# Optimization experiments

Measured on AMD Instinct MI355X. Metric: run time of the kernel, lower is better.

Reference implementation:

```python
import jax, jax.numpy as jnp
import numpy as np

WS = 8
NUM_HEADS = 4
DIM = 64
H = W = 128
B = 16
EPS = 1e-5


def _rel_pos_index(ws):
    coords = np.stack(np.meshgrid(np.arange(ws), np.arange(ws), indexing='ij'))  # (2,ws,ws)
    cf = coords.reshape(2, -1)
    rel = (cf[:, :, None] - cf[:, None, :]).transpose(1, 2, 0).astype(np.int64)
    rel[..., 0] += ws - 1
    rel[..., 1] += ws - 1
    rel[..., 0] *= 2 * ws - 1
    return jnp.asarray(rel.sum(-1))  # (ws*ws, ws*ws)

_RPI = _rel_pos_index(WS)


def _ln_hw(x, g, b):
    # LayerNorm over last two dims (H,W) of (B,C,H,W), affine shape (H,W)
    mu = x.mean(axis=(-2, -1), keepdims=True)
    var = ((x - mu) ** 2).mean(axis=(-2, -1), keepdims=True)
    return (x - mu) / jnp.sqrt(var + EPS) * g + b


def _ln_c(x, g, b):
    mu = x.mean(-1, keepdims=True)
    var = ((x - mu) ** 2).mean(-1, keepdims=True)
    return (x - mu) / jnp.sqrt(var + EPS) * g + b


def _win_part(x, ws):
    # (B,C,H,W) -> (B*nW, ws*ws, C)
    b, c, hh, ww = x.shape
    x = x.reshape(b, c, hh // ws, ws, ww // ws, ws)
    return x.transpose(0, 2, 4, 3, 5, 1).reshape(b * (hh // ws) * (ww // ws), ws * ws, c)


def _win_rev(w, ws, hh, ww, b):
    # (B*nW, ws*ws, C) -> (B,C,H,W)
    c = w.shape[-1]
    w = w.reshape(b, hh // ws, ww // ws, ws, ws, c)
    return w.transpose(0, 5, 1, 3, 2, 4).reshape(b, c, hh, ww)


def _forward(x, lclg1_ln1_g, lclg1_ln1_b, lclg1_conv_w, lclg1_conv_b, lclg1_ln2_g, lclg1_ln2_b,
             lclg2_ln1_g, lclg2_ln1_b, lclg2_conv_w, lclg2_conv_b, lclg2_ln2_g, lclg2_ln2_b,
             pos1, pos2, q_w, q_b, kv_w, kv_b, rpb_table, gamma, proj_w, proj_b,
             norm2_g, norm2_b, fc1_w, fc1_b, fc2_w, fc2_b):
    b, c, hh, ww = x.shape
    h = NUM_HEADS
    hd = c // h
    n = WS * WS
    scale = hd ** -0.5

    def lclg(z, g1, b1, cw, cb, g2, b2):
        z = _ln_hw(z, g1, b1)
        z = jnp.einsum('oc,bchw->bohw', cw, z) + cb[None, :, None, None]  # 1x1 conv
        return jax.nn.gelu(_ln_hw(z, g2, b2), approximate=False)

    x1 = lclg(x, lclg1_ln1_g, lclg1_ln1_b, lclg1_conv_w, lclg1_conv_b, lclg1_ln2_g, lclg1_ln2_b)
    x2 = lclg(x, lclg2_ln1_g, lclg2_ln1_b, lclg2_conv_w, lclg2_conv_b, lclg2_ln2_g, lclg2_ln2_b)

    x1w = _win_part(x1, WS) + pos1  # (B_, N, C)
    x2w = _win_part(x2, WS) + pos2
    bw = x1w.shape[0]

    q = (x1w @ q_w.T + q_b).reshape(bw, n, h, hd).transpose(0, 2, 1, 3) * scale  # (B_,h,N,hd)
    kv = (x2w @ kv_w.T + kv_b).reshape(bw, n, 2, h, hd).transpose(2, 0, 3, 1, 4)
    k, v = kv[0], kv[1]

    attn = jnp.einsum('bhnd,bhmd->bhnm', q, k)
    bias = rpb_table[_RPI.reshape(-1)].reshape(n, n, h).transpose(2, 0, 1)  # (h,N,N)
    attn = jax.nn.softmax(attn + bias[None], axis=-1)
    o = jnp.einsum('bhnm,bhmd->bhnd', attn, v)  # (B_,h,N,hd)

    # LAM_Module: attention over head_dim channels of (B_,h,N,hd)
    y = o.transpose(0, 3, 1, 2).reshape(bw, hd, h * n)  # (B_,hd,h*N)
    energy = jnp.einsum('bik,bjk->bij', y, y)  # (B_,hd,hd)
    lam = jnp.einsum('bij,bjk->bik', jax.nn.softmax(energy, axis=-1), y)
    y = (gamma * lam + y).reshape(bw, hd, h, n).transpose(0, 2, 3, 1)  # (B_,h,N,hd)

    xo = y.transpose(0, 2, 1, 3).reshape(bw, n, c) + q.transpose(0, 2, 1, 3).reshape(bw, n, c) + x1w
    xo = xo @ proj_w.T + proj_b

    xo = _win_rev(xo, WS, hh, ww, b)  # (B,C,H,W)

    # MLP with pre-norm residual over channel dim
    t = xo.reshape(b, c, hh * ww).transpose(0, 2, 1)  # (B,HW,C)
    tn = _ln_c(t, norm2_g, norm2_b)
    t = t + (jax.nn.gelu(tn @ fc1_w.T + fc1_b, approximate=False) @ fc2_w.T + fc2_b)
    return t.transpose(0, 2, 1).reshape(b, c, hh, ww)


def setup_inputs() -> dict:
    key = jax.random.key(0)
    ks = jax.random.split(key, 16)
    d = DIM

    def rn(i, shape, sc=0.02):
        return jax.random.normal(ks[i], shape, jnp.float32) * sc

    return dict(
        x=jax.random.normal(ks[0], (B, d, H, W), jnp.float32),
        lclg1_ln1_g=jnp.ones((H, W), jnp.float32), lclg1_ln1_b=jnp.zeros((H, W), jnp.float32),
        lclg1_conv_w=rn(1, (d, d)), lclg1_conv_b=jnp.zeros((d,), jnp.float32),
        lclg1_ln2_g=jnp.ones((H, W), jnp.float32), lclg1_ln2_b=jnp.zeros((H, W), jnp.float32),
        lclg2_ln1_g=jnp.ones((H, W), jnp.float32), lclg2_ln1_b=jnp.zeros((H, W), jnp.float32),
        lclg2_conv_w=rn(2, (d, d)), lclg2_conv_b=jnp.zeros((d,), jnp.float32),
        lclg2_ln2_g=jnp.ones((H, W), jnp.float32), lclg2_ln2_b=jnp.zeros((H, W), jnp.float32),
        pos1=jnp.ones((1, WS * WS, d), jnp.float32),
        pos2=jnp.ones((1, WS * WS, d), jnp.float32),
        q_w=rn(3, (d, d)), q_b=jnp.zeros((d,), jnp.float32),
        kv_w=rn(4, (2 * d, d)), kv_b=jnp.zeros((2 * d,), jnp.float32),
        rpb_table=rn(5, ((2 * WS - 1) ** 2, NUM_HEADS)),
        gamma=jnp.full((1,), 0.1, jnp.float32),
        proj_w=rn(6, (d, d)), proj_b=jnp.zeros((d,), jnp.float32),
        norm2_g=jnp.ones((d,), jnp.float32), norm2_b=jnp.zeros((d,), jnp.float32),
        fc1_w=rn(7, (d, d)), fc1_b=jnp.zeros((d,), jnp.float32),
        fc2_w=rn(8, (d, d)), fc2_b=jnp.zeros((d,), jnp.float32),
    )


def reference(x, lclg1_ln1_g, lclg1_ln1_b, lclg1_conv_w, lclg1_conv_b, lclg1_ln2_g, lclg1_ln2_b,
              lclg2_ln1_g, lclg2_ln1_b, lclg2_conv_w, lclg2_conv_b, lclg2_ln2_g, lclg2_ln2_b,
              pos1, pos2, q_w, q_b, kv_w, kv_b, rpb_table, gamma, proj_w, proj_b,
              norm2_g, norm2_b, fc1_w, fc1_b, fc2_w, fc2_b):
    return _forward(x, lclg1_ln1_g, lclg1_ln1_b, lclg1_conv_w, lclg1_conv_b, lclg1_ln2_g, lclg1_ln2_b,
                    lclg2_ln1_g, lclg2_ln1_b, lclg2_conv_w, lclg2_conv_b, lclg2_ln2_g, lclg2_ln2_b,
                    pos1, pos2, q_w, q_b, kv_w, kv_b, rpb_table, gamma, proj_w, proj_b,
                    norm2_g, norm2_b, fc1_w, fc1_b, fc2_w, fc2_b)
```

## Files before the change

kernel.cpp:

```cpp
#include <hip/hip_runtime.h>
#include <hip/hip_bf16.h>

typedef __hip_bfloat16 bf16;
typedef __attribute__((ext_vector_type(8))) short short8;
typedef __attribute__((ext_vector_type(4))) short short4v;
typedef __attribute__((ext_vector_type(4))) float float4v;
typedef __attribute__((ext_vector_type(2))) float float2v;

__device__ __forceinline__ short f2bs(float f){
    union { bf16 h; short s; } u; u.h = __float2bfloat16(f); return u.s;
}
__device__ __forceinline__ float bs2f(short s){
    return __uint_as_float(((unsigned)(unsigned short)s) << 16);
}
__device__ __forceinline__ float gelu_exact(float x){
    return 0.5f * x * (1.0f + erff(x * 0.70710678118654752440f));
}
#define MFMA(a,b,c) __builtin_amdgcn_mfma_f32_16x16x32_bf16((a),(b),(c),0,0,0)

#define HW 16384
#define NPLANE 1048576
#define EPS 1e-5f
#define LS 72

#define OFF_W1   0
#define OFF_W2   4096
#define OFF_QW   8192
#define OFF_KVW  12288
#define OFF_PW   20480
#define OFF_FW1  24576
#define OFF_FW2  28672

__global__ __launch_bounds__(256) void k_pre(const float* __restrict__ x,
                                             float* __restrict__ mu,
                                             float* __restrict__ rinv,
                                             const float* __restrict__ w1, const float* __restrict__ w2,
                                             const float* __restrict__ qw, const float* __restrict__ kvw,
                                             const float* __restrict__ pw, const float* __restrict__ fw1,
                                             const float* __restrict__ fw2,
                                             short* __restrict__ wb, float* __restrict__ rowsum){
    int bi = blockIdx.x;
    int tid = threadIdx.x;
    if (bi < 1024){
        const float* p = x + (size_t)bi * HW;
        float s = 0.f, ss = 0.f;
        for (int i = tid; i < HW/4; i += 256){
            float4v v = *(const float4v*)(p + i*4);
            #pragma unroll
            for (int k = 0; k < 4; k++){ s += v[k]; ss += v[k]*v[k]; }
        }
        __shared__ float rs[256], rss[256];
        rs[tid] = s; rss[tid] = ss; __syncthreads();
        for (int st = 128; st > 0; st >>= 1){
            if (tid < st){ rs[tid] += rs[tid+st]; rss[tid] += rss[tid+st]; }
            __syncthreads();
        }
        if (tid == 0){
            float m = rs[0] * (1.f/HW);
            float v = rss[0] * (1.f/HW) - m*m;
            mu[bi] = m; rinv[bi] = rsqrtf(v + EPS);
        }
    } else if (bi < 1032){
        int wi = bi - 1024;
        const float* src = wi==0?w1: wi==1?w2: wi==2?qw: wi==3?kvw: wi==4?(kvw+4096): wi==5?pw: wi==6?fw1: fw2;
        short* dst = wb + wi*4096;
        int base = tid*16;
        short8 o8[2];
        #pragma unroll
        for (int k = 0; k < 2; k++){
            float4v v0 = *(const float4v*)(src + base + 8*k);
            float4v v1 = *(const float4v*)(src + base + 8*k + 4);
            #pragma unroll
            for (int j = 0; j < 4; j++){ o8[k][j] = f2bs(v0[j]); o8[k][4+j] = f2bs(v1[j]); }
        }
        *(short8*)&dst[base]     = o8[0];
        *(short8*)&dst[base + 8] = o8[1];
    } else {
        if (tid < 128){
            int br = tid >> 6, o = tid & 63;
            const float* W = br ? w2 : w1;
            float s = 0.f;
            for (int c = 0; c < 64; c++) s += W[o*64 + c];
            rowsum[br*64 + o] = s;
        }
    }
}

__global__ __launch_bounds__(256) void k_conv(const float* __restrict__ x,
                                              const float* __restrict__ mu,
                                              const float* __restrict__ rinv,
                                              const float* __restrict__ g1a, const float* __restrict__ b1a,
                                              const float* __restrict__ cb1,
                                              const float* __restrict__ g1b, const float* __restrict__ b1b,
                                              const float* __restrict__ cb2,
                                              const short* __restrict__ wb,
                                              const float* __restrict__ rowsum,
                                              float* __restrict__ y1, float* __restrict__ w2g,
                                              float* __restrict__ partS, float* __restrict__ partQ){
    int blk = blockIdx.x;
    int b = blk >> 8; int tile = blk & 255; int hw0 = tile * 64;
    __shared__ __align__(16) short xn_bf[64*LS];
    const int tid = threadIdx.x;
    const int wq = tid >> 6, lane = tid & 63, qd = lane >> 4, col = lane & 15;
    const float4v zf = {0.f,0.f,0.f,0.f};

    {
        int p = tid & 63, cq = tid >> 6;
        const float* xb = x + (size_t)(b*64 + 16*cq)*HW + hw0 + p;
        float4v m4[4], r4[4];
        #pragma unroll
        for (int k = 0; k < 4; k++){
            m4[k] = *(const float4v*)(mu   + b*64 + 16*cq + 4*k);
            r4[k] = *(const float4v*)(rinv + b*64 + 16*cq + 4*k);
        }
        short8 o8[2];
        #pragma unroll
        for (int k = 0; k < 2; k++)
            #pragma unroll
            for (int j = 0; j < 8; j++){
                int jj = 8*k + j;
                float v = xb[(size_t)jj*HW];
                o8[k][j] = f2bs((v - m4[jj>>2][jj&3]) * r4[jj>>2][jj&3]);
            }
        *(short8*)&xn_bf[p*LS + 16*cq]     = o8[0];
        *(short8*)&xn_bf[p*LS + 16*cq + 8] = o8[1];
    }
    __syncthreads();

    #pragma unroll
    for (int br = 0; br < 2; br++){
        const short* W  = wb + (br ? OFF_W2 : OFF_W1);
        const float* cb = br ? cb2 : cb1;
        const float* gp = br ? g1b : g1a;
        const float* bp = br ? b1b : b1a;
        short8 a0 = *(const short8*)&W[(16*wq + col)*64 + 8*qd];
        short8 a1 = *(const short8*)&W[(16*wq + col)*64 + 32 + 8*qd];
        float cbv[4], rsv[4];
        #pragma unroll
        for (int r = 0; r < 4; r++){
            int o = 16*wq + 4*qd + r;
            cbv[r] = cb[o]; rsv[r] = rowsum[br*64 + o];
        }
        float sa[4]  = {0.f,0.f,0.f,0.f};
        float ssa[4] = {0.f,0.f,0.f,0.f};
        #pragma unroll
        for (int jn = 0; jn < 4; jn++){
            short8 bx0 = *(const short8*)&xn_bf[(16*jn + col)*LS + 8*qd];
            short8 bx1 = *(const short8*)&xn_bf[(16*jn + col)*LS + 32 + 8*qd];
            float4v acc = zf;
            acc = MFMA(a0, bx0, acc);
            acc = MFMA(a1, bx1, acc);
            int hw = hw0 + 16*jn + col;
            float gl = gp[hw], bl = bp[hw];
            float vals[4];
            #pragma unroll
            for (int r = 0; r < 4; r++){
                vals[r] = gl*acc[r] + bl*rsv[r] + cbv[r];
                sa[r]  += vals[r];
                ssa[r] += vals[r]*vals[r];
            }
            if (br == 0){
                #pragma unroll
                for (int r = 0; r < 4; r++)
                    y1[(size_t)(b*64 + 16*wq + 4*qd + r)*HW + hw] = vals[r];
            } else {
                int row = hw >> 7, cc = hw & 127;
                int win = (row >> 3)*16 + (cc >> 3);
                int t   = (row & 7)*8 + (cc & 7);
                float4v vv;
                #pragma unroll
                for (int r = 0; r < 4; r++) vv[r] = vals[r];
                *(float4v*)(w2g + ((size_t)(b*256 + win)*64 + t)*64 + 16*wq + 4*qd) = vv;
            }
        }
        #pragma unroll
        for (int r = 0; r < 4; r++){
            float s = sa[r], ss = ssa[r];
            s += __shfl_xor(s, 1); ss += __shfl_xor(ss, 1);
            s += __shfl_xor(s, 2); ss += __shfl_xor(ss, 2);
            s += __shfl_xor(s, 4); ss += __shfl_xor(ss, 4);
            s += __shfl_xor(s, 8); ss += __shfl_xor(ss, 8);
            if (col == 0){
                int o = 16*wq + 4*qd + r;
                size_t pi = ((size_t)(br*16 + b)*64 + o)*256 + tile;
                partS[pi] = s; partQ[pi] = ss;
            }
        }
    }
}

__global__ __launch_bounds__(256) void k_fin(const float* __restrict__ partS,
                                             const float* __restrict__ partQ,
                                             float* __restrict__ mu2,
                                             float* __restrict__ rinv2){
    int i = blockIdx.x*256 + threadIdx.x;
    const float* ps = partS + (size_t)i*256;
    const float* pq = partQ + (size_t)i*256;
    float s = 0.f, ss = 0.f;
    for (int k = 0; k < 64; k++){
        float4v a = *(const float4v*)(ps + k*4);
        float4v b = *(const float4v*)(pq + k*4);
        s += a[0]+a[1]+a[2]+a[3];
        ss += b[0]+b[1]+b[2]+b[3];
    }
    float m = s * (1.f/HW);
    float v = ss * (1.f/HW) - m*m;
    mu2[i] = m; rinv2[i] = rsqrtf(v + EPS);
}

__global__ __launch_bounds__(256, 4) void k_attn(float* __restrict__ x1, const float* __restrict__ w2g,
                                              const float* __restrict__ mu2, const float* __restrict__ rinv2,
                                              const float* __restrict__ g2a, const float* __restrict__ b2a,
                                              const float* __restrict__ g2b, const float* __restrict__ b2b,
                                              const float* __restrict__ pos1, const float* __restrict__ pos2,
                                              const short* __restrict__ wb,
                                              const float* __restrict__ qb, const float* __restrict__ kvb,
                                              const float* __restrict__ rpb, const float* __restrict__ gammap,
                                              const float* __restrict__ pb,
                                              const float* __restrict__ n2g, const float* __restrict__ n2b,
                                              const float* __restrict__ fb1,
                                              const float* __restrict__ fb2){
    int B = blockIdx.x;
    int hy = (B & 7) | ((B >> 5) & 8);
    int wx = (((B >> 9) & 7) << 1) | ((B >> 3) & 1);
    int b  = (B >> 4) & 15;
    int win = hy*16 + wx;

    const short* qwb  = wb + OFF_QW;
    const short* kvwb = wb + OFF_KVW;
    const short* pwb  = wb + OFF_PW;
    const short* f1b  = wb + OFF_FW1;
    const short* f2b  = wb + OFF_FW2;

    __shared__ __align__(16) char smem[40464];
    short* bufA = (short*)smem;
    short* bufK = (short*)(smem + 9216);
    short* bufV = (short*)(smem + 18432);
    short* bufQ = (short*)(smem + 27648);
    float* rpb_lds = (float*)(smem + 36864);
    float* energyS = (float*)(smem + 36864);
    short* soft_bf = (short*)(smem + 37888);
    float* XOf  = (float*)(smem + 18432);
    short* tnb  = (short*)smem;
    short* h1b  = (short*)(smem + 9216);
    float* sumS = (float*)(smem + 36864);
    float* sqS  = (float*)(smem + 37888);
    float* muS  = (float*)(smem + 38912);
    float* rinvS= (float*)(smem + 39168);

    const int tid = threadIdx.x;
    const int wq = tid >> 6, lane = tid & 63, qd = lane >> 4, col = lane & 15;
    size_t base = (size_t)b * NPLANE;
    #define HWOF(t) ((hy*8 + ((t)>>3))*128 + wx*8 + ((t)&7))

    const float4v zf = {0.f,0.f,0.f,0.f};
    const short8 zero8 = {0,0,0,0,0,0,0,0};

    for (int i = tid; i < 900; i += 256) rpb_lds[i] = rpb[i];

    {
        const float* src = w2g + ((size_t)(b*256 + win) << 12);
        int t = tid >> 2, c0 = (tid & 3) << 4;
        int hw = HWOF(t);
        float g = g2b[hw], lb = b2b[hw];
        const float* mup = mu2   + 1024 + b*64 + c0;
        const float* rvp = rinv2 + 1024 + b*64 + c0;
        short8 o8[2];
        #pragma unroll
        for (int k = 0; k < 4; k++){
            float4v v  = *(const float4v*)(src + (size_t)t*64 + c0 + 4*k);
            float4v m4 = *(const float4v*)(mup + 4*k);
            float4v r4 = *(const float4v*)(rvp + 4*k);
            float4v p4 = *(const float4v*)(pos2 + t*64 + c0 + 4*k);
            #pragma unroll
            for (int j = 0; j < 4; j++){
                float z = (v[j] - m4[j]) * r4[j] * g + lb;
                o8[k>>1][(k&1)*4 + j] = f2bs(gelu_exact(z) + p4[j]);
            }
        }
        *(short8*)&bufA[t*LS + c0]     = o8[0];
        *(short8*)&bufA[t*LS + c0 + 8] = o8[1];
    }
    __syncthreads();

    {
        short8 ax0 = *(const short8*)&bufA[(16*wq + col)*LS + 8*qd];
        short8 ax1 = *(const short8*)&bufA[(16*wq + col)*LS + 32 + 8*qd];
        #pragma unroll
        for (int jn = 0; jn < 4; jn++){
            int c = 16*jn + col;
            short8 wv0 = *(const short8*)&kvwb[(64 + c)*64 + 8*qd];
            short8 wv1 = *(const short8*)&kvwb[(64 + c)*64 + 32 + 8*qd];
            float4v acc = zf;
            acc = MFMA(ax0, wv0, acc);
            acc = MFMA(ax1, wv1, acc);
            float bv = kvb[64 + c];
            short4v pk;
            #pragma unroll
            for (int r = 0; r < 4; r++) pk[r] = f2bs(acc[r] + bv);
            *(short4v*)&bufV[c*LS + 16*wq + 4*qd] = pk;
        }
        short8 a0 = *(const short8*)&kvwb[(16*wq + col)*64 + 8*qd];
        short8 a1 = *(const short8*)&kvwb[(16*wq + col)*64 + 32 + 8*qd];
        float kbr[4];
        #pragma unroll
        for (int r = 0; r < 4; r++) kbr[r] = kvb[16*wq + 4*qd + r];
        #pragma unroll
        for (int jn = 0; jn < 4; jn++){
            int t = 16*jn + col;
            short8 bx0 = *(const short8*)&bufA[t*LS + 8*qd];
            short8 bx1 = *(const short8*)&bufA[t*LS + 32 + 8*qd];
            float4v acc = zf;
            acc = MFMA(a0, bx0, acc);
            acc = MFMA(a1, bx1, acc);
            short4v pk;
            #pragma unroll
            for (int r = 0; r < 4; r++) pk[r] = f2bs(acc[r] + kbr[r]);
            *(short4v*)&bufK[t*LS + 16*wq + 4*qd] = pk;
        }
    }
    __syncthreads();

    {
        int t = tid & 63, cq = tid >> 6;
        int hw = HWOF(t);
        float g = g2a[hw], lb = b2a[hw];
        const float* mup = mu2   + b*64 + 16*cq;
        const float* rvp = rinv2 + b*64 + 16*cq;
        float4v m4[4], r4[4], p4[4];
        #pragma unroll
        for (int k = 0; k < 4; k++){
            m4[k] = *(const float4v*)(mup + 4*k);
            r4[k] = *(const float4v*)(rvp + 4*k);
            p4[k] = *(const float4v*)(pos1 + t*64 + 16*cq + 4*k);
        }
        short8 o8[2];
        #pragma unroll
        for (int k = 0; k < 2; k++)
            #pragma unroll
            for (int j = 0; j < 8; j++){
                int jj = 8*k + j;
                float v = x1[base + (size_t)(16*cq + jj)*HW + hw];
                float z = (v - m4[jj>>2][jj&3]) * r4[jj>>2][jj&3] * g + lb;
                o8[k][j] = f2bs(gelu_exact(z) + p4[jj>>2][jj&3]);
            }
        *(short8*)&bufA[t*LS + 16*cq]     = o8[0];
        *(short8*)&bufA[t*LS + 16*cq + 8] = o8[1];
    }
    __syncthreads();

    {
        short8 a0 = *(const short8*)&qwb[(16*wq + col)*64 + 8*qd];
        short8 a1 = *(const short8*)&qwb[(16*wq + col)*64 + 32 + 8*qd];
        float qbr[4];
        #pragma unroll
        for (int r = 0; r < 4; r++) qbr[r] = qb[16*wq + 4*qd + r];
        #pragma unroll
        for (int jn = 0; jn < 4; jn++){
            int t = 16*jn + col;
            short8 bx0 = *(const short8*)&bufA[t*LS + 8*qd];
            short8 bx1 = *(const short8*)&bufA[t*LS + 32 + 8*qd];
            float4v acc = zf;
            acc = MFMA(a0, bx0, acc);
            acc = MFMA(a1, bx1, acc);
            short4v pk;
            #pragma unroll
            for (int r = 0; r < 4; r++) pk[r] = f2bs((acc[r] + qbr[r]) * 0.25f);
            *(short4v*)&bufQ[t*LS + 16*wq + 4*qd] = pk;
        }
    }
    short4v xreg[4];
    #pragma unroll
    for (int h = 0; h < 4; h++){
        short4v xr;
        #pragma unroll
        for (int r = 0; r < 4; r++)
            xr[r] = bufA[(16*wq + 4*qd + r)*LS + 16*h + col];
        xreg[h] = xr;
    }
    __syncthreads();

    int idx_t[4][4];
    {
        int t = 16*wq + col, ty = t >> 3, tx = t & 7;
        #pragma unroll
        for (int jn = 0; jn < 4; jn++)
            #pragma unroll
            for (int r = 0; r < 4; r++){
                int u = 16*jn + 4*qd + r;
                idx_t[jn][r] = (ty - (u>>3) + 7)*15 + (tx - (u&7) + 7);
            }
    }

    for (int h = 0; h < 4; h++){
        short8 bq = *(const short8*)&bufQ[(16*wq + col)*LS + h*16 + (qd & 1)*8];
        float pr[4][4];
        #pragma unroll
        for (int jn = 0; jn < 4; jn++){
            short8 ak = *(const short8*)&bufK[(16*jn + col)*LS + h*16 + (qd & 1)*8];
            if (qd >= 2) ak = zero8;
            float4v acc = MFMA(ak, bq, zf);
            #pragma unroll
            for (int r = 0; r < 4; r++)
                pr[jn][r] = acc[r] + rpb_lds[idx_t[jn][r]*4 + h];
        }
        float m = pr[0][0];
        #pragma unroll
        for (int jn = 0; jn < 4; jn++)
            #pragma unroll
            for (int r = 0; r < 4; r++) m = fmaxf(m, pr[jn][r]);
        m = fmaxf(m, __shfl_xor(m, 16));
        m = fmaxf(m, __shfl_xor(m, 32));
        float s = 0.f;
        #pragma unroll
        for (int jn = 0; jn < 4; jn++)
            #pragma unroll
            for (int r = 0; r < 4; r++){ pr[jn][r] = __expf(pr[jn][r] - m); s += pr[jn][r]; }
        s += __shfl_xor(s, 16);
        s += __shfl_xor(s, 32);
        float rc = 1.f / s;
        #pragma unroll
        for (int jn = 0; jn < 4; jn++){
            short4v pk;
            #pragma unroll
            for (int r = 0; r < 4; r++) pk[r] = f2bs(pr[jn][r] * rc);
            *(short4v*)&bufA[(16*wq + col)*LS + 16*jn + 4*qd] = pk;
        }
        short8 ap0 = *(const short8*)&bufA[(16*wq + col)*LS + 8*qd];
        short8 ap1 = *(const short8*)&bufA[(16*wq + col)*LS + 32 + 8*qd];
        short8 bv0 = *(const short8*)&bufV[(h*16 + col)*LS + 8*qd];
        short8 bv1 = *(const short8*)&bufV[(h*16 + col)*LS + 32 + 8*qd];
        float4v acc_o = zf;
        acc_o = MFMA(ap0, bv0, acc_o);
        acc_o = MFMA(ap1, bv1, acc_o);
        __syncthreads();
        short4v ot;
        #pragma unroll
        for (int r = 0; r < 4; r++) ot[r] = f2bs(acc_o[r]);
        *(short4v*)&bufV[(h*16 + col)*LS + 16*wq + 4*qd] = ot;
        #pragma unroll
        for (int r = 0; r < 4; r++)
            bufK[(16*wq + 4*qd + r)*LS + h*16 + col] = ot[r];
    }
    __syncthreads();

    {
        float4v acc_e = zf;
        #pragma unroll
        for (int h = 0; h < 4; h++){
            short8 f0 = *(const short8*)&bufV[(h*16 + col)*LS + 8*qd];
            short8 f1 = *(const short8*)&bufV[(h*16 + col)*LS + 32 + 8*qd];
            acc_e = MFMA(f0, f0, acc_e);
            acc_e = MFMA(f1, f1, acc_e);
        }
        if (wq == 0){
            #pragma unroll
            for (int r = 0; r < 4; r++) energyS[(4*qd + r)*16 + col] = acc_e[r];
        }
    }
    __syncthreads();
    if (tid < 16){
        int i = tid; float m = -1e30f;
        for (int j = 0; j < 16; j++) m = fmaxf(m, energyS[i*16 + j]);
        float s = 0.f; float e[16];
        for (int j = 0; j < 16; j++){ e[j] = __expf(energyS[i*16 + j] - m); s += e[j]; }
        float rc = 1.f / s;
        for (int j = 0; j < 16; j++) soft_bf[i*32 + j] = f2bs(e[j] * rc);
        for (int j = 0; j < 16; j++) soft_bf[i*32 + 16 + j] = 0;
    }
    __syncthreads();

    {
        float gam = gammap[0];
        short8 asf = *(const short8*)&soft_bf[col*32 + 8*qd];
        #pragma unroll
        for (int h = 0; h < 4; h++){
            short8 ay = *(const short8*)&bufK[(16*wq + col)*LS + 16*h + (qd & 1)*8];
            float4v acc = MFMA(ay, asf, zf);
            short4v xv = xreg[h];
            #pragma unroll
            for (int r = 0; r < 4; r++){
                int ro = (16*wq + 4*qd + r)*LS + 16*h + col;
                float ot = bs2f(bufK[ro]);
                float qv = bs2f(bufQ[ro]);
                float xo = gam*acc[r] + ot + qv + bs2f(xv[r]);
                bufK[ro] = f2bs(xo);
            }
        }
    }
    __syncthreads();

    {
        short8 a0 = *(const short8*)&pwb[(16*wq + col)*64 + 8*qd];
        short8 a1 = *(const short8*)&pwb[(16*wq + col)*64 + 32 + 8*qd];
        float pbr[4];
        #pragma unroll
        for (int r = 0; r < 4; r++) pbr[r] = pb[16*wq + 4*qd + r];
        #pragma unroll
        for (int jn = 0; jn < 4; jn++){
            int t = 16*jn + col;
            short8 bx0 = *(const short8*)&bufK[t*LS + 8*qd];
            short8 bx1 = *(const short8*)&bufK[t*LS + 32 + 8*qd];
            float4v acc = zf;
            acc = MFMA(a0, bx0, acc);
            acc = MFMA(a1, bx1, acc);
            float2v w0 = {acc[0]+pbr[0], acc[1]+pbr[1]};
            float2v w1 = {acc[2]+pbr[2], acc[3]+pbr[3]};
            *(float2v*)&XOf[t*66 + 16*wq + 4*qd]     = w0;
            *(float2v*)&XOf[t*66 + 16*wq + 4*qd + 2] = w1;
        }
    }
    __syncthreads();

    {
        int p = tid & 63, qg = tid >> 6;
        float s = 0.f, ss = 0.f;
        #pragma unroll
        for (int j = 0; j < 8; j++){
            float2v v = *(const float2v*)&XOf[p*66 + qg*16 + 2*j];
            s += v[0]+v[1]; ss += v[0]*v[0] + v[1]*v[1];
        }
        sumS[qg*64 + p] = s; sqS[qg*64 + p] = ss;
    }
    __syncthreads();
    if (tid < 64){
        float s  = sumS[tid] + sumS[64+tid] + sumS[128+tid] + sumS[192+tid];
        float ss = sqS[tid]  + sqS[64+tid]  + sqS[128+tid]  + sqS[192+tid];
        float m = s * (1.f/64.f);
        float var = ss * (1.f/64.f) - m*m;
        muS[tid] = m; rinvS[tid] = rsqrtf(var + EPS);
    }
    __syncthreads();
    {
        int p = tid & 63, qg = tid >> 6;
        float m = muS[p], rv = rinvS[p];
        short8 o8[2];
        #pragma unroll
        for (int k = 0; k < 2; k++)
            #pragma unroll
            for (int j = 0; j < 8; j++){
                int c = qg*16 + k*8 + j;
                o8[k][j] = f2bs((XOf[p*66 + c] - m) * rv * n2g[c] + n2b[c]);
            }
        *(short8*)&tnb[p*LS + qg*16]     = o8[0];
        *(short8*)&tnb[p*LS + qg*16 + 8] = o8[1];
    }
    __syncthreads();
    {
        short8 a0 = *(const short8*)&f1b[(16*wq + col)*64 + 8*qd];
        short8 a1 = *(const short8*)&f1b[(16*wq + col)*64 + 32 + 8*qd];
        float fbr[4];
        #pragma unroll
        for (int r = 0; r < 4; r++) fbr[r] = fb1[16*wq + 4*qd + r];
        #pragma unroll
        for (int jn = 0; jn < 4; jn++){
            int t = 16*jn + col;
            short8 bx0 = *(const short8*)&tnb[t*LS + 8*qd];
            short8 bx1 = *(const short8*)&tnb[t*LS + 32 + 8*qd];
            float4v acc = zf;
            acc = MFMA(a0, bx0, acc);
            acc = MFMA(a1, bx1, acc);
            short4v pk;
            #pragma unroll
            for (int r = 0; r < 4; r++) pk[r] = f2bs(gelu_exact(acc[r] + fbr[r]));
            *(short4v*)&h1b[t*LS + 16*wq + 4*qd] = pk;
        }
    }
    __syncthreads();
    {
        short8 a0 = *(const short8*)&h1b[(16*wq + col)*LS + 8*qd];
        short8 a1 = *(const short8*)&h1b[(16*wq + col)*LS + 32 + 8*qd];
        #pragma unroll
        for (int jn = 0; jn < 4; jn++){
            int c2 = 16*jn + col;
            short8 f0 = *(const short8*)&f2b[c2*64 + 8*qd];
            short8 f1 = *(const short8*)&f2b[c2*64 + 32 + 8*qd];
            float4v acc = zf;
            acc = MFMA(a0, f0, acc);
            acc = MFMA(a1, f1, acc);
            float bv = fb2[c2];
            float4v ov;
            #pragma unroll
            for (int r = 0; r < 4; r++)
                ov[r] = acc[r] + bv + XOf[(16*wq + 4*qd + r)*66 + c2];
            int t0 = 16*wq + 4*qd;
            *(float4v*)(x1 + base + (size_t)c2*HW + HWOF(t0)) = ov;
        }
    }
    #undef HWOF
}

extern "C" void kernel_launch(void* const* d_in, const int* in_sizes, int n_in,
                              void* d_out, int out_size, void* d_ws, size_t ws_size,
                              hipStream_t stream){
    const float* x        = (const float*)d_in[0];
    const float* l1_g1    = (const float*)d_in[1];
    const float* l1_b1    = (const float*)d_in[2];
    const float* l1_cw    = (const float*)d_in[3];
    const float* l1_cb    = (const float*)d_in[4];
    const float* l1_g2    = (const float*)d_in[5];
    const float* l1_b2    = (const float*)d_in[6];
    const float* l2_g1    = (const float*)d_in[7];
    const float* l2_b1    = (const float*)d_in[8];
    const float* l2_cw    = (const float*)d_in[9];
    const float* l2_cb    = (const float*)d_in[10];
    const float* l2_g2    = (const float*)d_in[11];
    const float* l2_b2    = (const float*)d_in[12];
    const float* pos1     = (const float*)d_in[13];
    const float* pos2     = (const float*)d_in[14];
    const float* q_w      = (const float*)d_in[15];
    const float* q_b      = (const float*)d_in[16];
    const float* kv_w     = (const float*)d_in[17];
    const float* kv_b     = (const float*)d_in[18];
    const float* rpb      = (const float*)d_in[19];
    const float* gamma    = (const float*)d_in[20];
    const float* proj_w   = (const float*)d_in[21];
    const float* proj_b   = (const float*)d_in[22];
    const float* norm2_g  = (const float*)d_in[23];
    const float* norm2_b  = (const float*)d_in[24];
    const float* fc1_w    = (const float*)d_in[25];
    const float* fc1_b    = (const float*)d_in[26];
    const float* fc2_w    = (const float*)d_in[27];
    const float* fc2_b    = (const float*)d_in[28];

    float* out = (float*)d_out;

    float* w2g   = (float*)d_ws;
    float* partS = w2g + (size_t)16*NPLANE;
    float* partQ = partS + (size_t)2048*256;
    float* mu1   = partQ + (size_t)2048*256;
    float* rinv1 = mu1 + 1024;
    float* mu2   = rinv1 + 1024;
    float* rinv2 = mu2 + 2048;
    float* rowsumG = rinv2 + 2048;
    short* wbuf  = (short*)(rowsumG + 128);

    k_pre  <<<1033, 256, 0, stream>>>(x, mu1, rinv1,
                                      l1_cw, l2_cw, q_w, kv_w, proj_w, fc1_w, fc2_w,
                                      wbuf, rowsumG);
    k_conv <<<4096, 256, 0, stream>>>(x, mu1, rinv1,
                                      l1_g1, l1_b1, l1_cb,
                                      l2_g1, l2_b1, l2_cb,
                                      wbuf, rowsumG,
                                      out, w2g, partS, partQ);
    k_fin  <<<8, 256, 0, stream>>>(partS, partQ, mu2, rinv2);
    k_attn <<<4096, 256, 0, stream>>>(out, w2g, mu2, rinv2,
                                      l1_g2, l1_b2, l2_g2, l2_b2,
                                      pos1, pos2, wbuf, q_b, kv_b,
                                      rpb, gamma, proj_b,
                                      norm2_g, norm2_b, fc1_b, fc2_b);
}
```

Before: 366.1 us.

## Recompute conv outputs inside attention kernel instead of storing intermediates

The conv kernel now only produces LayerNorm partial statistics and no longer writes the two 64-channel conv outputs (y1 into out, w2g windowed) to global memory. The attention kernel reloads x, normalizes it with the first LN stats, redoes both 1x1 convs with MFMA, and applies the second LN, GELU and positional add directly into LDS. This removes about 128 MB of intermediate writes and reads, at the cost of running the conv MFMAs twice and reading x twice. k_fin is also parallelised to one wave per row with shuffle reductions instead of one thread per row.

```diff
diff --git a/kernel.cpp b/kernel.cpp
--- a/kernel.cpp
+++ b/kernel.cpp
@@ -95,7 +95,6 @@
                                               const float* __restrict__ cb2,
                                               const short* __restrict__ wb,
                                               const float* __restrict__ rowsum,
-                                              float* __restrict__ y1, float* __restrict__ w2g,
                                               float* __restrict__ partS, float* __restrict__ partQ){
     int blk = blockIdx.x;
     int b = blk >> 8; int tile = blk & 255; int hw0 = tile * 64;
@@ -152,25 +151,11 @@
             acc = MFMA(a1, bx1, acc);
             int hw = hw0 + 16*jn + col;
             float gl = gp[hw], bl = bp[hw];
-            float vals[4];
             #pragma unroll
             for (int r = 0; r < 4; r++){
-                vals[r] = gl*acc[r] + bl*rsv[r] + cbv[r];
-                sa[r]  += vals[r];
-                ssa[r] += vals[r]*vals[r];
-            }
-            if (br == 0){
-                #pragma unroll
-                for (int r = 0; r < 4; r++)
-                    y1[(size_t)(b*64 + 16*wq + 4*qd + r)*HW + hw] = vals[r];
-            } else {
-                int row = hw >> 7, cc = hw & 127;
-                int win = (row >> 3)*16 + (cc >> 3);
-                int t   = (row & 7)*8 + (cc & 7);
-                float4v vv;
-                #pragma unroll
-                for (int r = 0; r < 4; r++) vv[r] = vals[r];
-                *(float4v*)(w2g + ((size_t)(b*256 + win)*64 + t)*64 + 16*wq + 4*qd) = vv;
+                float v = gl*acc[r] + bl*rsv[r] + cbv[r];
+                sa[r]  += v;
+                ssa[r] += v*v;
             }
         }
         #pragma unroll
@@ -193,22 +178,30 @@
                                              const float* __restrict__ partQ,
                                              float* __restrict__ mu2,
                                              float* __restrict__ rinv2){
-    int i = blockIdx.x*256 + threadIdx.x;
-    const float* ps = partS + (size_t)i*256;
-    const float* pq = partQ + (size_t)i*256;
-    float s = 0.f, ss = 0.f;
-    for (int k = 0; k < 64; k++){
-        float4v a = *(const float4v*)(ps + k*4);
-        float4v b = *(const float4v*)(pq + k*4);
-        s += a[0]+a[1]+a[2]+a[3];
-        ss += b[0]+b[1]+b[2]+b[3];
-    }
-    float m = s * (1.f/HW);
-    float v = ss * (1.f/HW) - m*m;
-    mu2[i] = m; rinv2[i] = rsqrtf(v + EPS);
-}
-
-__global__ __launch_bounds__(256, 4) void k_attn(float* __restrict__ x1, const float* __restrict__ w2g,
+    int row = blockIdx.x*4 + (threadIdx.x >> 6);
+    int lane = threadIdx.x & 63;
+    float4v a = *(const float4v*)(partS + (size_t)row*256 + lane*4);
+    float4v b = *(const float4v*)(partQ + (size_t)row*256 + lane*4);
+    float s  = a[0]+a[1]+a[2]+a[3];
+    float ss = b[0]+b[1]+b[2]+b[3];
+    #pragma unroll
+    for (int st = 1; st < 64; st <<= 1){
+        s  += __shfl_xor(s,  st);
+        ss += __shfl_xor(ss, st);
+    }
+    if (lane == 0){
+        float m = s * (1.f/HW);
+        float v = ss * (1.f/HW) - m*m;
+        mu2[row] = m; rinv2[row] = rsqrtf(v + EPS);
+    }
+}
+
+__global__ __launch_bounds__(256, 4) void k_attn(const float* __restrict__ x, float* __restrict__ outp,
+                                              const float* __restrict__ mu1, const float* __restrict__ rinv1,
+                                              const float* __restrict__ rowsum,
+                                              const float* __restrict__ cb1, const float* __restrict__ cb2,
+                                              const float* __restrict__ g1a, const float* __restrict__ b1a,
+                                              const float* __restrict__ g1b, const float* __restrict__ b1b,
                                               const float* __restrict__ mu2, const float* __restrict__ rinv2,
                                               const float* __restrict__ g2a, const float* __restrict__ b2a,
                                               const float* __restrict__ g2b, const float* __restrict__ b2b,
@@ -224,7 +217,6 @@
     int hy = (B & 7) | ((B >> 5) & 8);
     int wx = (((B >> 9) & 7) << 1) | ((B >> 3) & 1);
     int b  = (B >> 4) & 15;
-    int win = hy*16 + wx;
 
     const short* qwb  = wb + OFF_QW;
     const short* kvwb = wb + OFF_KVW;
@@ -259,33 +251,87 @@
     for (int i = tid; i < 900; i += 256) rpb_lds[i] = rpb[i];
 
     {
-        const float* src = w2g + ((size_t)(b*256 + win) << 12);
-        int t = tid >> 2, c0 = (tid & 3) << 4;
+        int t = tid & 63, cq = tid >> 6;
         int hw = HWOF(t);
-        float g = g2b[hw], lb = b2b[hw];
-        const float* mup = mu2   + 1024 + b*64 + c0;
-        const float* rvp = rinv2 + 1024 + b*64 + c0;
+        const float* mup = mu1   + b*64 + 16*cq;
+        const float* rvp = rinv1 + b*64 + 16*cq;
+        float4v m4[4], r4[4];
+        #pragma unroll
+        for (int k = 0; k < 4; k++){
+            m4[k] = *(const float4v*)(mup + 4*k);
+            r4[k] = *(const float4v*)(rvp + 4*k);
+        }
         short8 o8[2];
         #pragma unroll
-        for (int k = 0; k < 4; k++){
-            float4v v  = *(const float4v*)(src + (size_t)t*64 + c0 + 4*k);
-            float4v m4 = *(const float4v*)(mup + 4*k);
-            float4v r4 = *(const float4v*)(rvp + 4*k);
-            float4v p4 = *(const float4v*)(pos2 + t*64 + c0 + 4*k);
-            #pragma unroll
-            for (int j = 0; j < 4; j++){
-                float z = (v[j] - m4[j]) * r4[j] * g + lb;
-                o8[k>>1][(k&1)*4 + j] = f2bs(gelu_exact(z) + p4[j]);
-            }
-        }
-        *(short8*)&bufA[t*LS + c0]     = o8[0];
-        *(short8*)&bufA[t*LS + c0 + 8] = o8[1];
-    }
-    __syncthreads();
-
-    {
-        short8 ax0 = *(const short8*)&bufA[(16*wq + col)*LS + 8*qd];
-        short8 ax1 = *(const short8*)&bufA[(16*wq + col)*LS + 32 + 8*qd];
+        for (int k = 0; k < 2; k++)
+            #pragma unroll
+            for (int j = 0; j < 8; j++){
+                int jj = 8*k + j;
+                float v = x[base + (size_t)(16*cq + jj)*HW + hw];
+                o8[k][j] = f2bs((v - m4[jj>>2][jj&3]) * r4[jj>>2][jj&3]);
+            }
+        *(short8*)&bufV[t*LS + 16*cq]     = o8[0];
+        *(short8*)&bufV[t*LS + 16*cq + 8] = o8[1];
+    }
+    __syncthreads();
+
+    {
+        short8 a10 = *(const short8*)&wb[OFF_W1 + (16*wq + col)*64 + 8*qd];
+        short8 a11 = *(const short8*)&wb[OFF_W1 + (16*wq + col)*64 + 32 + 8*qd];
+        short8 a20 = *(const short8*)&wb[OFF_W2 + (16*wq + col)*64 + 8*qd];
+        short8 a21 = *(const short8*)&wb[OFF_W2 + (16*wq + col)*64 + 32 + 8*qd];
+        float cb1v[4], rs1v[4], m2a[4], rv2a[4];
+        float cb2v[4], rs2v[4], m2b[4], rv2b[4];
+        #pragma unroll
+        for (int r = 0; r < 4; r++){
+            int o = 16*wq + 4*qd + r;
+            cb1v[r] = cb1[o]; rs1v[r] = rowsum[o];
+            m2a[r] = mu2[b*64 + o]; rv2a[r] = rinv2[b*64 + o];
+            cb2v[r] = cb2[o]; rs2v[r] = rowsum[64 + o];
+            m2b[r] = mu2[1024 + b*64 + o]; rv2b[r] = rinv2[1024 + b*64 + o];
+        }
+        #pragma unroll
+        for (int jn = 0; jn < 4; jn++){
+            int t = 16*jn + col; int hw = HWOF(t);
+            short8 bx0 = *(const short8*)&bufV[t*LS + 8*qd];
+            short8 bx1 = *(const short8*)&bufV[t*LS + 32 + 8*qd];
+            {
+                float4v acc = zf;
+                acc = MFMA(a10, bx0, acc);
+                acc = MFMA(a11, bx1, acc);
+                float gl = g1a[hw], bl = b1a[hw], gg = g2a[hw], bo = b2a[hw];
+                float4v p4 = *(const float4v*)(pos1 + t*64 + 16*wq + 4*qd);
+                short4v pk;
+                #pragma unroll
+                for (int r = 0; r < 4; r++){
+                    float v = gl*acc[r] + bl*rs1v[r] + cb1v[r];
+                    float z = (v - m2a[r]) * rv2a[r] * gg + bo;
+                    pk[r] = f2bs(gelu_exact(z) + p4[r]);
+                }
+                *(short4v*)&bufA[t*LS + 16*wq + 4*qd] = pk;
+            }
+            {
+                float4v acc = zf;
+                acc = MFMA(a20, bx0, acc);
+                acc = MFMA(a21, bx1, acc);
+                float gl = g1b[hw], bl = b1b[hw], gg = g2b[hw], bo = b2b[hw];
+                float4v p4 = *(const float4v*)(pos2 + t*64 + 16*wq + 4*qd);
+                short4v pk;
+                #pragma unroll
+                for (int r = 0; r < 4; r++){
+                    float v = gl*acc[r] + bl*rs2v[r] + cb2v[r];
+                    float z = (v - m2b[r]) * rv2b[r] * gg + bo;
+                    pk[r] = f2bs(gelu_exact(z) + p4[r]);
+                }
+                *(short4v*)&bufQ[t*LS + 16*wq + 4*qd] = pk;
+            }
+        }
+    }
+    __syncthreads();
+
+    {
+        short8 ax0 = *(const short8*)&bufQ[(16*wq + col)*LS + 8*qd];
+        short8 ax1 = *(const short8*)&bufQ[(16*wq + col)*LS + 32 + 8*qd];
         #pragma unroll
         for (int jn = 0; jn < 4; jn++){
             int c = 16*jn + col;
@@ -308,8 +354,8 @@
         #pragma unroll
         for (int jn = 0; jn < 4; jn++){
             int t = 16*jn + col;
-            short8 bx0 = *(const short8*)&bufA[t*LS + 8*qd];
-            short8 bx1 = *(const short8*)&bufA[t*LS + 32 + 8*qd];
+            short8 bx0 = *(const short8*)&bufQ[t*LS + 8*qd];
+            short8 bx1 = *(const short8*)&bufQ[t*LS + 32 + 8*qd];
             float4v acc = zf;
             acc = MFMA(a0, bx0, acc);
             acc = MFMA(a1, bx1, acc);
@@ -318,34 +364,6 @@
             for (int r = 0; r < 4; r++) pk[r] = f2bs(acc[r] + kbr[r]);
             *(short4v*)&bufK[t*LS + 16*wq + 4*qd] = pk;
         }
-    }
-    __syncthreads();
-
-    {
-        int t = tid & 63, cq = tid >> 6;
-        int hw = HWOF(t);
-        float g = g2a[hw], lb = b2a[hw];
-        const float* mup = mu2   + b*64 + 16*cq;
-        const float* rvp = rinv2 + b*64 + 16*cq;
-        float4v m4[4], r4[4], p4[4];
-        #pragma unroll
-        for (int k = 0; k < 4; k++){
-            m4[k] = *(const float4v*)(mup + 4*k);
-            r4[k] = *(const float4v*)(rvp + 4*k);
-            p4[k] = *(const float4v*)(pos1 + t*64 + 16*cq + 4*k);
-        }
-        short8 o8[2];
-        #pragma unroll
-        for (int k = 0; k < 2; k++)
-            #pragma unroll
-            for (int j = 0; j < 8; j++){
-                int jj = 8*k + j;
-                float v = x1[base + (size_t)(16*cq + jj)*HW + hw];
-                float z = (v - m4[jj>>2][jj&3]) * r4[jj>>2][jj&3] * g + lb;
-                o8[k][j] = f2bs(gelu_exact(z) + p4[jj>>2][jj&3]);
-            }
-        *(short8*)&bufA[t*LS + 16*cq]     = o8[0];
-        *(short8*)&bufA[t*LS + 16*cq + 8] = o8[1];
     }
     __syncthreads();
 
@@ -584,7 +602,7 @@
             for (int r = 0; r < 4; r++)
                 ov[r] = acc[r] + bv + XOf[(16*wq + 4*qd + r)*66 + c2];
             int t0 = 16*wq + 4*qd;
-            *(float4v*)(x1 + base + (size_t)c2*HW + HWOF(t0)) = ov;
+            *(float4v*)(outp + base + (size_t)c2*HW + HWOF(t0)) = ov;
         }
     }
     #undef HWOF
@@ -625,8 +643,7 @@
 
     float* out = (float*)d_out;
 
-    float* w2g   = (float*)d_ws;
-    float* partS = w2g + (size_t)16*NPLANE;
+    float* partS = (float*)d_ws;
     float* partQ = partS + (size_t)2048*256;
     float* mu1   = partQ + (size_t)2048*256;
     float* rinv1 = mu1 + 1024;
@@ -642,9 +659,12 @@
                                       l1_g1, l1_b1, l1_cb,
                                       l2_g1, l2_b1, l2_cb,
                                       wbuf, rowsumG,
-                                      out, w2g, partS, partQ);
-    k_fin  <<<8, 256, 0, stream>>>(partS, partQ, mu2, rinv2);
-    k_attn <<<4096, 256, 0, stream>>>(out, w2g, mu2, rinv2,
+                                      partS, partQ);
+    k_fin  <<<512, 256, 0, stream>>>(partS, partQ, mu2, rinv2);
+    k_attn <<<4096, 256, 0, stream>>>(x, out, mu1, rinv1, rowsumG,
+                                      l1_cb, l2_cb,
+                                      l1_g1, l1_b1, l2_g1, l2_b1,
+                                      mu2, rinv2,
                                       l1_g2, l1_b2, l2_g2, l2_b2,
                                       pos1, pos2, wbuf, q_b, kv_b,
                                       rpb, gamma, proj_b,
```

Result: faster. 322.9 us (-11.8%).
